# Optimization experiments

Hardware: AMD Instinct MI355X
Metric: run time of the kernel (lower is better)

The kernel has to match this reference:

```python
import jax, jax.numpy as jnp
import numpy as np

KC = 32      # cluster_num
KS = 3       # kernel_size
AREA = KS * KS
ITERS = 10   # KMeans Lloyd iterations (fixed, deterministic init)


def _unfold3(x):
    # torch nn.Unfold(kernel_size=3, padding=1): feature dim ordered cin-major, area-minor
    b, c, h, w = x.shape
    xp = jnp.pad(x, ((0, 0), (0, 0), (1, 1), (1, 1)))
    cols = jnp.stack([xp[:, :, i:i + h, j:j + w] for i in range(KS) for j in range(KS)], axis=2)  # [b,c,area,h,w]
    return cols.reshape(b, c * AREA, h * w).transpose(0, 2, 1)  # [b, hw, c*area]


def _kmeans_assign(feat):
    # Lloyd's KMeans on [s, d] features; deterministic strided init; returns [s] int assignments
    s, d = feat.shape
    c0 = feat[jnp.arange(KC) * (s // KC)]
    f2 = (feat * feat).sum(-1, keepdims=True)
    def dists(c):
        return f2 - 2.0 * feat @ c.T + (c * c).sum(-1)[None, :]
    def step(c, _):
        idx = jnp.argmin(dists(c), axis=1)
        cnt = jax.ops.segment_sum(jnp.ones((s,), feat.dtype), idx, KC)
        sm = jax.ops.segment_sum(feat, idx, KC)
        c_new = jnp.where(cnt[:, None] > 0, sm / jnp.maximum(cnt, 1.0)[:, None], c)
        return c_new, None
    c, _ = jax.lax.scan(step, c0, None, length=ITERS)
    return jnp.argmin(dists(c), axis=1)


def _seg_mean(p, idx):
    # per-cluster mean of patches -> patch-space centroids [K, f]
    s = p.shape[0]
    cnt = jax.ops.segment_sum(jnp.ones((s,), p.dtype), idx, KC)
    return jax.ops.segment_sum(p, idx, KC) / jnp.maximum(cnt, 1.0)[:, None]


def _mlp2(x, W1, b1, W2, b2):
    return jax.nn.relu(jax.nn.relu(x @ W1 + b1) @ W2 + b2)


def setup_inputs():
    key = jax.random.key(0)
    ks = jax.random.split(key, 16)
    cin, cout, m = 32, 32, 16
    f = cin * AREA
    g = lambda k, shp, sc: jax.random.normal(k, shp, dtype=jnp.float32) * sc
    return {
        "x": g(ks[0], (4, cin, 64, 64), 1.0),
        "Wh1": g(ks[1], (f, m), (2.0 / f) ** 0.5), "bh1": jnp.zeros((m,), jnp.float32),
        "Wh2": g(ks[2], (m, m), (2.0 / m) ** 0.5), "bh2": jnp.zeros((m,), jnp.float32),
        "Wa": g(ks[3], (m, AREA), (2.0 / m) ** 0.5), "ba": jnp.zeros((AREA,), jnp.float32),
        "Wc": g(ks[4], (m, cin), (2.0 / m) ** 0.5), "bc": jnp.zeros((cin,), jnp.float32),
        "Wo": g(ks[5], (m, cout), (2.0 / m) ** 0.5), "bo": jnp.zeros((cout,), jnp.float32),
        "kernels": g(ks[6], (cin, AREA, cout), (2.0 / (cin * AREA)) ** 0.5),
        "Wb1": g(ks[7], (f, m), (2.0 / f) ** 0.5), "bb1": jnp.zeros((m,), jnp.float32),
        "Wb2": g(ks[8], (m, m), (2.0 / m) ** 0.5), "bb2": jnp.zeros((m,), jnp.float32),
        "Wb3": g(ks[9], (m, cout), (2.0 / m) ** 0.5), "bb3": jnp.zeros((cout,), jnp.float32),
    }


def reference(x, Wh1, bh1, Wh2, bh2, Wa, ba, Wc, bc, Wo, bo, kernels, Wb1, bb1, Wb2, bb2, Wb3, bb3):
    b, cin, h, w = x.shape
    s = h * w
    cout = kernels.shape[-1]
    patches = _unfold3(x)                                        # [b, s, cin*area]
    feat = patches.reshape(b, s, cin, AREA).mean(-1)             # cluster_source='channel'
    idx = jax.vmap(_kmeans_assign)(jax.lax.stop_gradient(feat))  # [b, s] cluster assignments
    centroids = jax.vmap(_seg_mean)(patches, idx)                # [b, K, cin*area]
    # low_rank kernel generator: rank-1 modulation along cin/area/cout of shared base kernel
    kf = _mlp2(centroids, Wh1, bh1, Wh2, bh2)                    # [b, K, m]
    w_cin = jax.nn.sigmoid(kf @ Wc + bc)                         # [b, K, cin]
    w_area = jax.nn.sigmoid(kf @ Wa + ba)                        # [b, K, area]
    w_cout = jax.nn.sigmoid(kf @ Wo + bo)                        # [b, K, cout]
    kern = (w_cin[:, :, :, None, None] * w_area[:, :, None, :, None]
            * w_cout[:, :, None, None, :] * kernels[None, None])  # [b, K, cin, area, cout]
    kern = kern.reshape(b, KC, cin * AREA, cout)
    bias = _mlp2(centroids, Wb1, bb1, Wb2, bb2) @ Wb3 + bb3      # [b, K, cout] (bias='cluster')
    # gather per-pixel kernel/bias by cluster id, grouped matmul, scatter back (dense-gather form)
    bi = jnp.arange(b)[:, None]
    Wpix = kern[bi, idx]                                         # [b, s, f, cout]
    out = jnp.einsum('bsf,bsfo->bso', patches, Wpix) + bias[bi, idx]
    return out.reshape(b, h, w, cout).transpose(0, 3, 1, 2), idx
```

## Files before the change

### kernel.cpp

```cpp
#include <hip/hip_runtime.h>
#include <stdint.h>

typedef unsigned long long u64;

#define Bn 4
#define CINn 32
#define Hn 64
#define Wn 64
#define Sn 4096
#define KCn 32
#define Mn 16
#define COUTn 32
#define AREAn 9
#define Fn 288
#define NITER 10
#define FXSCALE 4294967296.0
#define NBLK_B 16
#define PXB 256
#define CMAX 160
#define LDK 292
#define NFLAG ((NITER + 2) * Bn * NBLK_B)

#define AT_LD_U32(p)    __hip_atomic_load((p),  __ATOMIC_RELAXED, __HIP_MEMORY_SCOPE_AGENT)
#define AT_LD_U64(p)    __hip_atomic_load((p),  __ATOMIC_RELAXED, __HIP_MEMORY_SCOPE_AGENT)
#define AT_ST_U32(p,v)  __hip_atomic_store((p), (v), __ATOMIC_RELAXED, __HIP_MEMORY_SCOPE_AGENT)
#define AT_ST_U64(p,v)  __hip_atomic_store((p), (v), __ATOMIC_RELAXED, __HIP_MEMORY_SCOPE_AGENT)

static __device__ __forceinline__ float relu_(float v){ return v > 0.f ? v : 0.f; }
static __device__ __forceinline__ float sigmoid_(float v){ return 1.f / (1.f + expf(-v)); }

__global__ __launch_bounds__(256) void k_init(const float* __restrict__ x,
                                              float* __restrict__ feat,
                                              u64* __restrict__ gsum,
                                              unsigned* __restrict__ gcnt,
                                              unsigned* __restrict__ flags){
    int g = blockIdx.x * 256 + threadIdx.x;
    if (g < 3 * Bn * KCn * CINn) gsum[g] = 0ull;
    if (g < 3 * Bn * KCn)        gcnt[g] = 0u;
    if (g < NFLAG)               flags[g] = 0u;
    int p = g & (Sn - 1);
    int c = (g >> 12) & (CINn - 1);
    int b = g >> 17;
    int y = p >> 6, xx = p & 63;
    const float* xc = x + ((size_t)(b * CINn + c) << 12);
    float s = 0.f;
    #pragma unroll
    for (int i = 0; i < 3; ++i){
        int yy = y + i - 1;
        if (yy < 0 || yy >= Hn) continue;
        #pragma unroll
        for (int j = 0; j < 3; ++j){
            int xj = xx + j - 1;
            if (xj < 0 || xj >= Wn) continue;
            s += xc[(yy << 6) + xj];
        }
    }
    feat[g] = s * (1.f / 9.f);
}

struct AssignSh {
    float4 fvQ[8][PXB];
    float  f2L[PXB];
    float4 cent4[KCn][8];
    float  c2[KCn];
    float  bestdM[4][PXB];
    int    bestkM[4][PXB];
    unsigned lcnt[KCn];
    unsigned off32[KCn + 1];
    unsigned scat[KCn];
    unsigned cntPrev[KCn];
    int   plist[PXB];
    int   rankF[PXB];
    unsigned baseBT[KCn];
};
struct SmkSh {
    float psum[CINn][AREAn][8];
    float centL[Fn];
    int   pl[256];
    float part1[16][16], part2[16][16];
    float hL[2][Mn];
    float kfL[2][Mn];
};
union ShU { AssignSh a; SmkSh m; };

__global__ __launch_bounds__(256) void k_main(const float* __restrict__ x,
        const float* __restrict__ feat,
        u64* __restrict__ gsum, unsigned* __restrict__ gcnt,
        unsigned* __restrict__ blkcnt,
        int* __restrict__ idx, float* __restrict__ idxf,
        int* __restrict__ sorted, int4* __restrict__ chunk_map,
        const float* __restrict__ Wh1, const float* __restrict__ bh1,
        const float* __restrict__ Wh2, const float* __restrict__ bh2,
        const float* __restrict__ Wa,  const float* __restrict__ ba,
        const float* __restrict__ Wc,  const float* __restrict__ bc,
        const float* __restrict__ Wo,  const float* __restrict__ bo,
        const float* __restrict__ Wb1, const float* __restrict__ bb1,
        const float* __restrict__ Wb2, const float* __restrict__ bb2,
        const float* __restrict__ Wb3, const float* __restrict__ bb3,
        float* __restrict__ wcin, float* __restrict__ warea,
        float* __restrict__ wcout, float* __restrict__ biasb,
        unsigned* __restrict__ flg){
    __shared__ int bi256[PXB];
    __shared__ unsigned totK[KCn];
    __shared__ unsigned goffK[KCn + 1];
    __shared__ ShU sh;

    const int tid  = threadIdx.x;
    const int b    = blockIdx.x >> 4;
    const int tnum = blockIdx.x & 15;
    const int p    = tnum * PXB + tid;
    const int kq   = tid >> 6;
    const int pxb  = tid & 63;

    #pragma unroll
    for (int cq = 0; cq < 8; ++cq){
        float4 v;
        v.x = feat[(b * CINn + cq * 4 + 0) * Sn + p];
        v.y = feat[(b * CINn + cq * 4 + 1) * Sn + p];
        v.z = feat[(b * CINn + cq * 4 + 2) * Sn + p];
        v.w = feat[(b * CINn + cq * 4 + 3) * Sn + p];
        sh.a.fvQ[cq][tid] = v;
    }
    __syncthreads();
    {
        float s = 0.f;
        #pragma unroll
        for (int cq = 0; cq < 8; ++cq){
            float4 v = sh.a.fvQ[cq][tid];
            s = fmaf(v.x, v.x, s); s = fmaf(v.y, v.y, s);
            s = fmaf(v.z, v.z, s); s = fmaf(v.w, v.w, s);
        }
        sh.a.f2L[tid] = s;
    }

    for (int iter = 0; iter <= NITER; ++iter){
        const int prev = (iter + 2) % 3;
        const int cur  = iter % 3;
        const int nxt  = (iter + 1) % 3;

        if (iter == 0){
            float* centf = (float*)sh.a.cent4;
            for (int e = tid; e < KCn * CINn; e += 256){
                int k = e >> 5, c = e & 31;
                centf[k * 32 + c] = feat[(b * CINn + c) * Sn + k * (Sn / KCn)];
            }
        } else {
            if (tid < NBLK_B)
                while (AT_LD_U32(&flg[(iter - 1) * Bn * NBLK_B + b * NBLK_B + tid]) == 0u)
                    __builtin_amdgcn_s_sleep(2);
            __syncthreads();
            if (tid < KCn)
                sh.a.cntPrev[tid] = AT_LD_U32(&gcnt[(prev * Bn + b) * KCn + tid]);
            u64 sv[4];
            #pragma unroll
            for (int q = 0; q < 4; ++q)
                sv[q] = AT_LD_U64(&gsum[(size_t)(prev * Bn + b) * KCn * CINn + tid + q * 256]);
            __syncthreads();
            float* centf = (float*)sh.a.cent4;
            #pragma unroll
            for (int q = 0; q < 4; ++q){
                int e = tid + q * 256;
                int k = e >> 5, c = e & 31;
                unsigned cn = sh.a.cntPrev[k];
                if (cn > 0)
                    centf[k * 32 + c] = (float)((double)(long long)sv[q] / ((double)cn * FXSCALE));
            }
        }
        if (iter < NITER && tnum == 0){
            for (int e = tid; e < KCn * CINn; e += 256)
                AT_ST_U64(&gsum[(size_t)(nxt * Bn + b) * KCn * CINn + e], 0ull);
            if (tid < KCn) AT_ST_U32(&gcnt[(nxt * Bn + b) * KCn + tid], 0u);
        }
        __syncthreads();
        if (tid < KCn){
            const float4* cr = sh.a.cent4[tid];
            float s = 0.f;
            #pragma unroll
            for (int cq2 = 0; cq2 < 8; ++cq2){
                float4 v = cr[cq2];
                s = fmaf(v.x, v.x, s); s = fmaf(v.y, v.y, s);
                s = fmaf(v.z, v.z, s); s = fmaf(v.w, v.w, s);
            }
            sh.a.c2[tid] = s;
            sh.a.lcnt[tid] = 0u;
            sh.a.scat[tid] = 0u;
        }
        __syncthreads();

        float dot[4][8];
        #pragma unroll
        for (int j = 0; j < 4; ++j)
            #pragma unroll
            for (int kk = 0; kk < 8; ++kk) dot[j][kk] = 0.f;
        #pragma unroll
        for (int cq2 = 0; cq2 < 8; ++cq2){
            float4 fr0 = sh.a.fvQ[cq2][pxb];
            float4 fr1 = sh.a.fvQ[cq2][pxb + 64];
            float4 fr2 = sh.a.fvQ[cq2][pxb + 128];
            float4 fr3 = sh.a.fvQ[cq2][pxb + 192];
            #pragma unroll
            for (int kk = 0; kk < 8; ++kk){
                float4 cv = sh.a.cent4[kq * 8 + kk][cq2];
                dot[0][kk] = fmaf(fr0.x, cv.x, dot[0][kk]); dot[0][kk] = fmaf(fr0.y, cv.y, dot[0][kk]);
                dot[0][kk] = fmaf(fr0.z, cv.z, dot[0][kk]); dot[0][kk] = fmaf(fr0.w, cv.w, dot[0][kk]);
                dot[1][kk] = fmaf(fr1.x, cv.x, dot[1][kk]); dot[1][kk] = fmaf(fr1.y, cv.y, dot[1][kk]);
                dot[1][kk] = fmaf(fr1.z, cv.z, dot[1][kk]); dot[1][kk] = fmaf(fr1.w, cv.w, dot[1][kk]);
                dot[2][kk] = fmaf(fr2.x, cv.x, dot[2][kk]); dot[2][kk] = fmaf(fr2.y, cv.y, dot[2][kk]);
                dot[2][kk] = fmaf(fr2.z, cv.z, dot[2][kk]); dot[2][kk] = fmaf(fr2.w, cv.w, dot[2][kk]);
                dot[3][kk] = fmaf(fr3.x, cv.x, dot[3][kk]); dot[3][kk] = fmaf(fr3.y, cv.y, dot[3][kk]);
                dot[3][kk] = fmaf(fr3.z, cv.z, dot[3][kk]); dot[3][kk] = fmaf(fr3.w, cv.w, dot[3][kk]);
            }
        }
        #pragma unroll
        for (int j = 0; j < 4; ++j){
            const int px = pxb + 64 * j;
            const float f2v = sh.a.f2L[px];
            float bd = 3.402823466e38f; int bkk = kq * 8;
            #pragma unroll
            for (int kk = 0; kk < 8; ++kk){
                float d = f2v - 2.f * dot[j][kk] + sh.a.c2[kq * 8 + kk];
                if (d < bd){ bd = d; bkk = kq * 8 + kk; }
            }
            sh.a.bestdM[kq][px] = bd;
            sh.a.bestkM[kq][px] = bkk;
        }
        __syncthreads();
        int bk;
        {
            float bd = sh.a.bestdM[0][tid]; bk = sh.a.bestkM[0][tid];
            #pragma unroll
            for (int q = 1; q < 4; ++q){
                float d2 = sh.a.bestdM[q][tid];
                if (d2 < bd){ bd = d2; bk = sh.a.bestkM[q][tid]; }
            }
            bi256[tid] = bk;
        }

        if (iter < NITER){
            atomicAdd(&sh.a.lcnt[bk], 1u);
            __syncthreads();
            if (tid == 0){
                unsigned acc = 0;
                #pragma unroll
                for (int k = 0; k < KCn; ++k){ sh.a.off32[k] = acc; acc += sh.a.lcnt[k]; }
                sh.a.off32[KCn] = acc;
            }
            __syncthreads();
            {
                unsigned pos = sh.a.off32[bk] + atomicAdd(&sh.a.scat[bk], 1u);
                sh.a.plist[pos] = tid;
            }
            __syncthreads();
            {
                const int wv   = tid >> 6;
                const int lane = tid & 63;
                const int hf   = lane >> 5;
                const int c    = lane & 31;
                const float* fvf = (const float*)sh.a.fvQ;
                #pragma unroll
                for (int kq2 = 0; kq2 < 8; ++kq2){
                    const int k  = wv * 8 + kq2;
                    const int o0 = (int)sh.a.off32[k];
                    const int n  = (int)sh.a.off32[k + 1] - o0;
                    u64 acc = 0ull;
                    for (int i = hf; i < n; i += 2){
                        int px = sh.a.plist[o0 + i];
                        float fvv = fvf[(c >> 2) * 1024 + px * 4 + (c & 3)];
                        acc += (u64)llrint((double)fvv * FXSCALE);
                    }
                    acc += __shfl_down(acc, 32);
                    if (lane < 32 && n > 0)
                        atomicAdd(&gsum[(size_t)(cur * Bn + b) * KCn * CINn + k * CINn + c], acc);
                }
            }
            if (tid < KCn){
                unsigned v = sh.a.lcnt[tid];
                if (v) atomicAdd(&gcnt[(cur * Bn + b) * KCn + tid], v);
            }
            __syncthreads();
            if (tid == 0)
                AT_ST_U32(&flg[iter * Bn * NBLK_B + b * NBLK_B + tnum], 1u);
        } else {
            idx [b * Sn + p] = bk;
            idxf[b * Sn + p] = (float)bk;
            __syncthreads();
            if (tid < KCn){
                int r = 0;
                for (int q = 0; q < PXB; ++q)
                    if (bi256[q] == tid) sh.a.rankF[q] = r++;
                AT_ST_U32(&blkcnt[(b * KCn + tid) * NBLK_B + tnum], (unsigned)r);
            }
            __syncthreads();
            if (tid == 0)
                AT_ST_U32(&flg[NITER * Bn * NBLK_B + b * NBLK_B + tnum], 1u);
        }
    }

    if (tid < NBLK_B)
        while (AT_LD_U32(&flg[NITER * Bn * NBLK_B + b * NBLK_B + tid]) == 0u)
            __builtin_amdgcn_s_sleep(2);
    __syncthreads();
    if (tid < KCn){
        unsigned run = 0, mybase = 0;
        #pragma unroll 4
        for (int blk = 0; blk < NBLK_B; ++blk){
            unsigned v = AT_LD_U32(&blkcnt[(b * KCn + tid) * NBLK_B + blk]);
            if (blk == tnum) mybase = run;
            run += v;
        }
        totK[tid] = run;
        sh.a.baseBT[tid] = mybase;
    }
    __syncthreads();
    if (tid == 0){
        unsigned acc = 0;
        #pragma unroll
        for (int k = 0; k < KCn; ++k){ goffK[k] = acc; acc += totK[k]; }
        goffK[KCn] = acc;
    }
    __syncthreads();
    {
        int k = bi256[tid];
        unsigned pos = goffK[k] + sh.a.baseBT[k] + (unsigned)sh.a.rankF[tid];
        AT_ST_U32((unsigned*)&sorted[b * Sn + pos], (unsigned)p);
    }
    if (tnum == 0 && tid == 0){
        int j = 0;
        for (int k = 0; k < KCn; ++k){
            int n = (int)totK[k];
            for (int cb = 0; cb < n; cb += 32){
                chunk_map[b * CMAX + j] = make_int4(k, (int)goffK[k] + cb, min(32, n - cb), 0);
                ++j;
            }
        }
        for (; j < CMAX; ++j) chunk_map[b * CMAX + j] = make_int4(-1, 0, 0, 0);
    }
    __syncthreads();
    if (tid == 0)
        AT_ST_U32(&flg[(NITER + 1) * Bn * NBLK_B + b * NBLK_B + tnum], 1u);
    if (tid < NBLK_B)
        while (AT_LD_U32(&flg[(NITER + 1) * Bn * NBLK_B + b * NBLK_B + tid]) == 0u)
            __builtin_amdgcn_s_sleep(2);
    __syncthreads();

    for (int kq2 = 0; kq2 < 2; ++kq2){
        const int kk   = tnum * 2 + kq2;
        const int off0 = (int)goffK[kk];
        const int nmy  = (int)totK[kk];
        __syncthreads();
        {
            const int cA = tid >> 3;
            const int s  = tid & 7;
            const float* xc = x + ((size_t)(b * CINn + cA) << 12);
            float acc[9];
            #pragma unroll
            for (int a = 0; a < 9; ++a) acc[a] = 0.f;
            for (int base = 0; base < nmy; base += 256){
                int m = min(256, nmy - base);
                __syncthreads();
                if (tid < m)
                    sh.m.pl[tid] = (int)AT_LD_U32((unsigned*)&sorted[b * Sn + off0 + base + tid]);
                __syncthreads();
                #pragma unroll 2
                for (int i = s; i < m; i += 8){
                    int pp = sh.m.pl[i];
                    int py = pp >> 6, px2 = pp & 63;
                    #pragma unroll
                    for (int a = 0; a < 9; ++a){
                        int y1 = py + a / 3 - 1, x1 = px2 + (a % 3) - 1;
                        float v = (y1 >= 0 && y1 < Hn && x1 >= 0 && x1 < Wn)
                                  ? xc[(y1 << 6) + x1] : 0.f;
                        acc[a] += v;
                    }
                }
            }
            __syncthreads();
            #pragma unroll
            for (int a = 0; a < 9; ++a) sh.m.psum[cA][a][s] = acc[a];
            __syncthreads();
            float invn = 1.f / (float)max(nmy, 1);
            for (int f = tid; f < Fn; f += 256){
                int c = f / 9, a = f - c * 9;
                float sm = 0.f;
                #pragma unroll
                for (int s2 = 0; s2 < 8; ++s2) sm += sh.m.psum[c][a][s2];
                sh.m.centL[f] = sm * invn;
            }
        }
        __syncthreads();
        {
            int j = tid & 15, rep = tid >> 4;
            float p1 = 0.f, p2 = 0.f;
            int fbeg = rep * 18;
            for (int ff = fbeg; ff < fbeg + 18; ++ff){
                float cv = sh.m.centL[ff];
                p1 = fmaf(cv, Wh1[ff * Mn + j], p1);
                p2 = fmaf(cv, Wb1[ff * Mn + j], p2);
            }
            sh.m.part1[rep][j] = p1;
            sh.m.part2[rep][j] = p2;
        }
        __syncthreads();
        if (tid < 32){
            int br = tid >> 4, j = tid & 15;
            float s = br ? bb1[j] : bh1[j];
            for (int r = 0; r < 16; ++r) s += br ? sh.m.part2[r][j] : sh.m.part1[r][j];
            sh.m.hL[br][j] = relu_(s);
        }
        __syncthreads();
        if (tid < 32){
            int br = tid >> 4, j = tid & 15;
            const float* W2 = br ? Wb2 : Wh2;
            float s = br ? bb2[j] : bh2[j];
            #pragma unroll
            for (int i = 0; i < Mn; ++i) s = fmaf(sh.m.hL[br][i], W2[i * Mn + j], s);
            sh.m.kfL[br][j] = relu_(s);
        }
        __syncthreads();
        if (tid < 32){
            int o = tid;
            float s1 = bc[o], s2 = bo[o], s3 = bb3[o];
            #pragma unroll
            for (int i = 0; i < Mn; ++i){
                float kv = sh.m.kfL[0][i];
                s1 = fmaf(kv, Wc[i * COUTn + o], s1);
                s2 = fmaf(kv, Wo[i * COUTn + o], s2);
                s3 = fmaf(sh.m.kfL[1][i], Wb3[i * COUTn + o], s3);
            }
            wcin [(b * KCn + kk) * CINn  + o] = sigmoid_(s1);
            wcout[(b * KCn + kk) * COUTn + o] = sigmoid_(s2);
            biasb[(b * KCn + kk) * COUTn + o] = s3;
        } else if (tid < 41){
            int a2 = tid - 32;
            float s = ba[a2];
            #pragma unroll
            for (int i = 0; i < Mn; ++i) s = fmaf(sh.m.kfL[0][i], Wa[i * AREAn + a2], s);
            warea[(b * KCn + kk) * AREAn + a2] = sigmoid_(s);
        }
    }
}

__global__ __launch_bounds__(256) void k_out(const float* __restrict__ x,
                                             const int* __restrict__ sorted,
                                             const int4* __restrict__ chunk_map,
                                             const float* __restrict__ wcin,
                                             const float* __restrict__ warea,
                                             const float* __restrict__ wcout,
                                             const float* __restrict__ biasb,
                                             const float* __restrict__ kern0,
                                             float* __restrict__ out){
    const int b   = blockIdx.x / CMAX;
    const int j   = blockIdx.x - b * CMAX;
    const int tid = threadIdx.x;

    int4 cm = chunk_map[b * CMAX + j];
    const int kcur = cm.x;
    if (kcur < 0) return;
    const int base = cm.y;
    const int cnt  = cm.z;

    __shared__ float kernT[COUTn * LDK];
    __shared__ float patchL[32 * LDK];
    __shared__ int   pix[32];
    __shared__ float wcl[CINn], wal[AREAn], wol[COUTn], biasL[COUTn];

    if (tid < 32){
        pix[tid] = (tid < cnt) ? sorted[b * Sn + base + tid] : -1;
    } else if (tid < 64)  wcl[tid - 32]    = wcin [(b * KCn + kcur) * CINn  + tid - 32];
    else if (tid < 96)    wol[tid - 64]    = wcout[(b * KCn + kcur) * COUTn + tid - 64];
    else if (tid < 105)   wal[tid - 96]    = warea[(b * KCn + kcur) * AREAn + tid - 96];
    else if (tid >= 128 && tid < 160) biasL[tid - 128] = biasb[(b * KCn + kcur) * COUTn + tid - 128];

    const int fA = tid;       const int cA = fA / 9, aA = fA - cA * 9;
    const int dyA = aA / 3 - 1, dxA = aA % 3 - 1;
    const int fB = 256 + tid; const int cB = fB / 9, aB = fB - cB * 9;
    const int dyB = aB / 3 - 1, dxB = aB % 3 - 1;
    __syncthreads();

    {
        int o  = tid >> 3;
        int q  = tid & 7;
        int f0 = q * 36;
        int cc = q * 4, aa = 0;
        float wo_ = wol[o];
        float* kr = kernT + o * LDK + f0;
        #pragma unroll 4
        for (int i2 = 0; i2 < 36; ++i2){
            kr[i2] = wcl[cc] * wal[aa] * wo_ * kern0[(f0 + i2) * COUTn + o];
            if (++aa == 9){ aa = 0; ++cc; }
        }
    }

    #pragma unroll 4
    for (int px = 0; px < 32; ++px){
        int pp = pix[px];
        float vA = 0.f, vB = 0.f;
        if (pp >= 0){
            int py = pp >> 6, pxx = pp & 63;
            int y1 = py + dyA, x1 = pxx + dxA;
            if (y1 >= 0 && y1 < Hn && x1 >= 0 && x1 < Wn)
                vA = x[((size_t)(b * CINn + cA) << 12) + (y1 << 6) + x1];
            if (tid < 32){
                int y2 = py + dyB, x2 = pxx + dxB;
                if (y2 >= 0 && y2 < Hn && x2 >= 0 && x2 < Wn)
                    vB = x[((size_t)(b * CINn + cB) << 12) + (y2 << 6) + x2];
            }
        }
        patchL[px * LDK + tid] = vA;
        if (tid < 32) patchL[px * LDK + 256 + tid] = vB;
    }
    __syncthreads();

    const int o2 = tid & 15, p2 = tid >> 4;
    const int oA = o2 * 2, oB = o2 * 2 + 1;
    const int pxA = p2 * 2, pxB = p2 * 2 + 1;
    const bool actA = pxA < cnt, actB = pxB < cnt;
    if (!actA && !actB) return;

    const float* krA = kernT + oA * LDK;
    const float* krB = kernT + oB * LDK;
    const float* prA = patchL + pxA * LDK;
    const float* prB = patchL + pxB * LDK;
    float s00 = 0.f, s01 = 0.f, s10 = 0.f, s11 = 0.f;
    #pragma unroll 4
    for (int fq = 0; fq < Fn; fq += 4){
        float4 k0 = *reinterpret_cast<const float4*>(krA + fq);
        float4 k1 = *reinterpret_cast<const float4*>(krB + fq);
        float4 pa = *reinterpret_cast<const float4*>(prA + fq);
        float4 pb = *reinterpret_cast<const float4*>(prB + fq);
        s00 = fmaf(pa.x,k0.x,s00); s00 = fmaf(pa.y,k0.y,s00); s00 = fmaf(pa.z,k0.z,s00); s00 = fmaf(pa.w,k0.w,s00);
        s01 = fmaf(pa.x,k1.x,s01); s01 = fmaf(pa.y,k1.y,s01); s01 = fmaf(pa.z,k1.z,s01); s01 = fmaf(pa.w,k1.w,s01);
        s10 = fmaf(pb.x,k0.x,s10); s10 = fmaf(pb.y,k0.y,s10); s10 = fmaf(pb.z,k0.z,s10); s10 = fmaf(pb.w,k0.w,s10);
        s11 = fmaf(pb.x,k1.x,s11); s11 = fmaf(pb.y,k1.y,s11); s11 = fmaf(pb.z,k1.z,s11); s11 = fmaf(pb.w,k1.w,s11);
    }
    if (actA){
        int pp = pix[pxA];
        out[((size_t)(b * COUTn + oA) << 12) + pp] = biasL[oA] + s00;
        out[((size_t)(b * COUTn + oB) << 12) + pp] = biasL[oB] + s01;
    }
    if (actB){
        int pp = pix[pxB];
        out[((size_t)(b * COUTn + oA) << 12) + pp] = biasL[oA] + s10;
        out[((size_t)(b * COUTn + oB) << 12) + pp] = biasL[oB] + s11;
    }
}

extern "C" void kernel_launch(void* const* d_in, const int* in_sizes, int n_in,
                              void* d_out, int out_size, void* d_ws, size_t ws_size,
                              hipStream_t stream){
    const float* x    = (const float*)d_in[0];
    const float* Wh1  = (const float*)d_in[1];
    const float* bh1  = (const float*)d_in[2];
    const float* Wh2  = (const float*)d_in[3];
    const float* bh2  = (const float*)d_in[4];
    const float* Wa   = (const float*)d_in[5];
    const float* ba   = (const float*)d_in[6];
    const float* Wc   = (const float*)d_in[7];
    const float* bc   = (const float*)d_in[8];
    const float* Wo   = (const float*)d_in[9];
    const float* bo   = (const float*)d_in[10];
    const float* kern0= (const float*)d_in[11];
    const float* Wb1  = (const float*)d_in[12];
    const float* bb1  = (const float*)d_in[13];
    const float* Wb2  = (const float*)d_in[14];
    const float* bb2  = (const float*)d_in[15];
    const float* Wb3  = (const float*)d_in[16];
    const float* bb3  = (const float*)d_in[17];

    char* ws = (char*)d_ws;
    float*    feat   = (float*)(ws + 0);
    u64*      gsum   = (u64*)  (ws + 2097152);
    unsigned* gcnt   = (unsigned*)(ws + 2195456);
    unsigned* blkcnt = (unsigned*)(ws + 2196992);
    int*      idx    = (int*)  (ws + 2205184);
    int*      sorted = (int*)  (ws + 2270720);
    float*    wcin   = (float*)(ws + 2336256);
    float*    warea  = (float*)(ws + 2352640);
    float*    wcout  = (float*)(ws + 2357248);
    float*    biasb  = (float*)(ws + 2373632);
    int4*     chunk_map = (int4*)(ws + 2390016);
    unsigned* flags  = (unsigned*)(ws + 2400256);

    float* outp = (float*)d_out;
    float* idxf = outp + (size_t)Bn * COUTn * Sn;

    k_init<<<(Bn * CINn * Sn) / 256, 256, 0, stream>>>(x, feat, gsum, gcnt, flags);
    k_main<<<Bn * NBLK_B, 256, 0, stream>>>(x, feat, gsum, gcnt, blkcnt, idx, idxf,
                                            sorted, chunk_map,
                                            Wh1, bh1, Wh2, bh2, Wa, ba, Wc, bc, Wo, bo,
                                            Wb1, bb1, Wb2, bb2, Wb3, bb3,
                                            wcin, warea, wcout, biasb, flags);
    k_out<<<Bn * CMAX, 256, 0, stream>>>(x, sorted, chunk_map, wcin, warea, wcout,
                                         biasb, kern0, outp);
}
```

Before: 230.9 us.

## Replace global atomics with per-block slots and leader-reduced centroids in KMeans loop

KMeans partial sums are no longer atomically added into shared global accumulators. Each block now writes its own slot, and block 0 of each batch reduces the slots, computes the centroids and their norms, then publishes them behind a flag for the other blocks. Patch-space centroid sums are load-balanced by splitting sorted pixel runs across all blocks, with float atomics into a global buffer. The change also adds a padded transposed feature copy in LDS to avoid bank conflicts, and changes the output tile thread mapping. This removes atomic contention, but adds an extra serial leader step and an extra barrier per iteration, and float atomics make the result order-dependent.

```diff
diff --git a/kernel.cpp b/kernel.cpp
--- a/kernel.cpp
+++ b/kernel.cpp
@@ -19,7 +19,13 @@
 #define PXB 256
 #define CMAX 160
 #define LDK 292
-#define NFLAG ((NITER + 2) * Bn * NBLK_B)
+
+#define FL_PUB(it)  ((it)*64)
+#define FL_CENT(it) (640 + (it)*4)
+#define FL_SORT  680
+#define FL_SCAT  744
+#define FL_SEG   808
+#define NFLAGS   1024
 
 #define AT_LD_U32(p)    __hip_atomic_load((p),  __ATOMIC_RELAXED, __HIP_MEMORY_SCOPE_AGENT)
 #define AT_LD_U64(p)    __hip_atomic_load((p),  __ATOMIC_RELAXED, __HIP_MEMORY_SCOPE_AGENT)
@@ -31,13 +37,11 @@
 
 __global__ __launch_bounds__(256) void k_init(const float* __restrict__ x,
                                               float* __restrict__ feat,
-                                              u64* __restrict__ gsum,
-                                              unsigned* __restrict__ gcnt,
+                                              float* __restrict__ gpsum,
                                               unsigned* __restrict__ flags){
     int g = blockIdx.x * 256 + threadIdx.x;
-    if (g < 3 * Bn * KCn * CINn) gsum[g] = 0ull;
-    if (g < 3 * Bn * KCn)        gcnt[g] = 0u;
-    if (g < NFLAG)               flags[g] = 0u;
+    if (g < Bn * KCn * Fn) gpsum[g] = 0.f;
+    if (g < NFLAGS)        flags[g] = 0u;
     int p = g & (Sn - 1);
     int c = (g >> 12) & (CINn - 1);
     int b = g >> 17;
@@ -60,6 +64,7 @@
 
 struct AssignSh {
     float4 fvQ[8][PXB];
+    float  fvP[PXB][33];
     float  f2L[PXB];
     float4 cent4[KCn][8];
     float  c2[KCn];
@@ -68,15 +73,17 @@
     unsigned lcnt[KCn];
     unsigned off32[KCn + 1];
     unsigned scat[KCn];
-    unsigned cntPrev[KCn];
-    int   plist[PXB];
-    int   rankF[PXB];
+    unsigned cntTot[KCn];
+    int    plist[PXB];
+    int    rankF[PXB];
     unsigned baseBT[KCn];
 };
 struct SmkSh {
     float psum[CINn][AREAn][8];
     float centL[Fn];
-    int   pl[256];
+    int   spl[PXB];
+    int   runK[33], runS[33], runE[33];
+    int   nruns;
     float part1[16][16], part2[16][16];
     float hL[2][Mn];
     float kfL[2][Mn];
@@ -85,9 +92,10 @@
 
 __global__ __launch_bounds__(256) void k_main(const float* __restrict__ x,
         const float* __restrict__ feat,
-        u64* __restrict__ gsum, unsigned* __restrict__ gcnt,
+        u64* __restrict__ bslot, unsigned* __restrict__ slotCnt,
+        float* __restrict__ centG, float* __restrict__ c2G,
         unsigned* __restrict__ blkcnt,
-        int* __restrict__ idx, float* __restrict__ idxf,
+        float* __restrict__ idxf,
         int* __restrict__ sorted, int4* __restrict__ chunk_map,
         const float* __restrict__ Wh1, const float* __restrict__ bh1,
         const float* __restrict__ Wh2, const float* __restrict__ bh2,
@@ -99,6 +107,7 @@
         const float* __restrict__ Wb3, const float* __restrict__ bb3,
         float* __restrict__ wcin, float* __restrict__ warea,
         float* __restrict__ wcout, float* __restrict__ biasb,
+        float* __restrict__ gpsum,
         unsigned* __restrict__ flg){
     __shared__ int bi256[PXB];
     __shared__ unsigned totK[KCn];
@@ -112,6 +121,7 @@
     const int kq   = tid >> 6;
     const int pxb  = tid & 63;
 
+    float fv[CINn];
     #pragma unroll
     for (int cq = 0; cq < 8; ++cq){
         float4 v;
@@ -120,71 +130,99 @@
         v.z = feat[(b * CINn + cq * 4 + 2) * Sn + p];
         v.w = feat[(b * CINn + cq * 4 + 3) * Sn + p];
         sh.a.fvQ[cq][tid] = v;
-    }
-    __syncthreads();
+        fv[cq * 4 + 0] = v.x; fv[cq * 4 + 1] = v.y;
+        fv[cq * 4 + 2] = v.z; fv[cq * 4 + 3] = v.w;
+    }
     {
         float s = 0.f;
         #pragma unroll
-        for (int cq = 0; cq < 8; ++cq){
-            float4 v = sh.a.fvQ[cq][tid];
-            s = fmaf(v.x, v.x, s); s = fmaf(v.y, v.y, s);
-            s = fmaf(v.z, v.z, s); s = fmaf(v.w, v.w, s);
-        }
+        for (int c = 0; c < CINn; ++c) s = fmaf(fv[c], fv[c], s);
         sh.a.f2L[tid] = s;
-    }
+        #pragma unroll
+        for (int c = 0; c < CINn; ++c) sh.a.fvP[tid][c] = fv[c];
+    }
+    __syncthreads();
 
     for (int iter = 0; iter <= NITER; ++iter){
-        const int prev = (iter + 2) % 3;
-        const int cur  = iter % 3;
-        const int nxt  = (iter + 1) % 3;
-
         if (iter == 0){
             float* centf = (float*)sh.a.cent4;
             for (int e = tid; e < KCn * CINn; e += 256){
                 int k = e >> 5, c = e & 31;
-                centf[k * 32 + c] = feat[(b * CINn + c) * Sn + k * (Sn / KCn)];
-            }
+                centf[e] = feat[(b * CINn + c) * Sn + k * (Sn / KCn)];
+            }
+            __syncthreads();
+            if (tid < KCn){
+                const float4* cr = sh.a.cent4[tid];
+                float s = 0.f;
+                #pragma unroll
+                for (int cq2 = 0; cq2 < 8; ++cq2){
+                    float4 v = cr[cq2];
+                    s = fmaf(v.x, v.x, s); s = fmaf(v.y, v.y, s);
+                    s = fmaf(v.z, v.z, s); s = fmaf(v.w, v.w, s);
+                }
+                sh.a.c2[tid] = s;
+            }
+        } else if (tnum == 0){
+            if (tid < NBLK_B)
+                while (AT_LD_U32(&flg[FL_PUB(iter - 1) + b * 16 + tid]) == 0u)
+                    __builtin_amdgcn_s_sleep(2);
+            __syncthreads();
+            u64 s4[4] = {0ull, 0ull, 0ull, 0ull};
+            #pragma unroll
+            for (int q = 0; q < 4; ++q){
+                const int e = tid + q * 256;
+                #pragma unroll
+                for (int blk = 0; blk < NBLK_B; ++blk)
+                    s4[q] += AT_LD_U64(&bslot[(size_t)(b * NBLK_B + blk) * 1024 + e]);
+            }
+            if (tid < KCn){
+                unsigned ct = 0;
+                #pragma unroll
+                for (int blk = 0; blk < NBLK_B; ++blk)
+                    ct += AT_LD_U32(&slotCnt[(b * NBLK_B + blk) * KCn + tid]);
+                sh.a.cntTot[tid] = ct;
+            }
+            __syncthreads();
+            float* centf = (float*)sh.a.cent4;
+            #pragma unroll
+            for (int q = 0; q < 4; ++q){
+                const int e = tid + q * 256;
+                const int k = e >> 5;
+                unsigned cn = sh.a.cntTot[k];
+                if (cn > 0)
+                    centf[e] = (float)((double)(long long)s4[q] / ((double)cn * FXSCALE));
+                AT_ST_U32((unsigned*)&centG[b * 1024 + e], __float_as_uint(centf[e]));
+            }
+            __syncthreads();
+            if (tid < KCn){
+                const float4* cr = sh.a.cent4[tid];
+                float s = 0.f;
+                #pragma unroll
+                for (int cq2 = 0; cq2 < 8; ++cq2){
+                    float4 v = cr[cq2];
+                    s = fmaf(v.x, v.x, s); s = fmaf(v.y, v.y, s);
+                    s = fmaf(v.z, v.z, s); s = fmaf(v.w, v.w, s);
+                }
+                sh.a.c2[tid] = s;
+                AT_ST_U32((unsigned*)&c2G[b * KCn + tid], __float_as_uint(s));
+            }
+            __syncthreads();
+            if (tid == 0) AT_ST_U32(&flg[FL_CENT(iter - 1) + b], 1u);
         } else {
-            if (tid < NBLK_B)
-                while (AT_LD_U32(&flg[(iter - 1) * Bn * NBLK_B + b * NBLK_B + tid]) == 0u)
+            if (tid == 0)
+                while (AT_LD_U32(&flg[FL_CENT(iter - 1) + b]) == 0u)
                     __builtin_amdgcn_s_sleep(2);
             __syncthreads();
+            float* centf = (float*)sh.a.cent4;
+            #pragma unroll
+            for (int q = 0; q < 4; ++q){
+                const int e = tid + q * 256;
+                centf[e] = __uint_as_float(AT_LD_U32((unsigned*)&centG[b * 1024 + e]));
+            }
             if (tid < KCn)
-                sh.a.cntPrev[tid] = AT_LD_U32(&gcnt[(prev * Bn + b) * KCn + tid]);
-            u64 sv[4];
-            #pragma unroll
-            for (int q = 0; q < 4; ++q)
-                sv[q] = AT_LD_U64(&gsum[(size_t)(prev * Bn + b) * KCn * CINn + tid + q * 256]);
-            __syncthreads();
-            float* centf = (float*)sh.a.cent4;
-            #pragma unroll
-            for (int q = 0; q < 4; ++q){
-                int e = tid + q * 256;
-                int k = e >> 5, c = e & 31;
-                unsigned cn = sh.a.cntPrev[k];
-                if (cn > 0)
-                    centf[k * 32 + c] = (float)((double)(long long)sv[q] / ((double)cn * FXSCALE));
-            }
-        }
-        if (iter < NITER && tnum == 0){
-            for (int e = tid; e < KCn * CINn; e += 256)
-                AT_ST_U64(&gsum[(size_t)(nxt * Bn + b) * KCn * CINn + e], 0ull);
-            if (tid < KCn) AT_ST_U32(&gcnt[(nxt * Bn + b) * KCn + tid], 0u);
-        }
-        __syncthreads();
-        if (tid < KCn){
-            const float4* cr = sh.a.cent4[tid];
-            float s = 0.f;
-            #pragma unroll
-            for (int cq2 = 0; cq2 < 8; ++cq2){
-                float4 v = cr[cq2];
-                s = fmaf(v.x, v.x, s); s = fmaf(v.y, v.y, s);
-                s = fmaf(v.z, v.z, s); s = fmaf(v.w, v.w, s);
-            }
-            sh.a.c2[tid] = s;
-            sh.a.lcnt[tid] = 0u;
-            sh.a.scat[tid] = 0u;
-        }
+                sh.a.c2[tid] = __uint_as_float(AT_LD_U32((unsigned*)&c2G[b * KCn + tid]));
+        }
+        if (tid < KCn){ sh.a.lcnt[tid] = 0u; sh.a.scat[tid] = 0u; }
         __syncthreads();
 
         float dot[4][8];
@@ -256,7 +294,6 @@
                 const int lane = tid & 63;
                 const int hf   = lane >> 5;
                 const int c    = lane & 31;
-                const float* fvf = (const float*)sh.a.fvQ;
                 #pragma unroll
                 for (int kq2 = 0; kq2 < 8; ++kq2){
                     const int k  = wv * 8 + kq2;
@@ -265,23 +302,18 @@
                     u64 acc = 0ull;
                     for (int i = hf; i < n; i += 2){
                         int px = sh.a.plist[o0 + i];
-                        float fvv = fvf[(c >> 2) * 1024 + px * 4 + (c & 3)];
-                        acc += (u64)llrint((double)fvv * FXSCALE);
+                        acc += (u64)llrint((double)sh.a.fvP[px][c] * FXSCALE);
                     }
                     acc += __shfl_down(acc, 32);
-                    if (lane < 32 && n > 0)
-                        atomicAdd(&gsum[(size_t)(cur * Bn + b) * KCn * CINn + k * CINn + c], acc);
+                    if (lane < 32)
+                        AT_ST_U64(&bslot[(size_t)(b * NBLK_B + tnum) * 1024 + k * 32 + c], acc);
                 }
             }
-            if (tid < KCn){
-                unsigned v = sh.a.lcnt[tid];
-                if (v) atomicAdd(&gcnt[(cur * Bn + b) * KCn + tid], v);
-            }
-            __syncthreads();
-            if (tid == 0)
-                AT_ST_U32(&flg[iter * Bn * NBLK_B + b * NBLK_B + tnum], 1u);
+            if (tid < KCn)
+                AT_ST_U32(&slotCnt[(b * NBLK_B + tnum) * KCn + tid], sh.a.lcnt[tid]);
+            __syncthreads();
+            if (tid == 0) AT_ST_U32(&flg[FL_PUB(iter) + b * 16 + tnum], 1u);
         } else {
-            idx [b * Sn + p] = bk;
             idxf[b * Sn + p] = (float)bk;
             __syncthreads();
             if (tid < KCn){
@@ -291,13 +323,12 @@
                 AT_ST_U32(&blkcnt[(b * KCn + tid) * NBLK_B + tnum], (unsigned)r);
             }
             __syncthreads();
-            if (tid == 0)
-                AT_ST_U32(&flg[NITER * Bn * NBLK_B + b * NBLK_B + tnum], 1u);
+            if (tid == 0) AT_ST_U32(&flg[FL_SORT + b * 16 + tnum], 1u);
         }
     }
 
     if (tid < NBLK_B)
-        while (AT_LD_U32(&flg[NITER * Bn * NBLK_B + b * NBLK_B + tid]) == 0u)
+        while (AT_LD_U32(&flg[FL_SORT + b * 16 + tid]) == 0u)
             __builtin_amdgcn_s_sleep(2);
     __syncthreads();
     if (tid < KCn){
@@ -322,7 +353,7 @@
     {
         int k = bi256[tid];
         unsigned pos = goffK[k] + sh.a.baseBT[k] + (unsigned)sh.a.rankF[tid];
-        AT_ST_U32((unsigned*)&sorted[b * Sn + pos], (unsigned)p);
+        AT_ST_U32((unsigned*)&sorted[b * Sn + pos], (unsigned)(p | (k << 16)));
     }
     if (tnum == 0 && tid == 0){
         int j = 0;
@@ -336,57 +367,84 @@
         for (; j < CMAX; ++j) chunk_map[b * CMAX + j] = make_int4(-1, 0, 0, 0);
     }
     __syncthreads();
-    if (tid == 0)
-        AT_ST_U32(&flg[(NITER + 1) * Bn * NBLK_B + b * NBLK_B + tnum], 1u);
+    if (tid == 0) AT_ST_U32(&flg[FL_SCAT + b * 16 + tnum], 1u);
     if (tid < NBLK_B)
-        while (AT_LD_U32(&flg[(NITER + 1) * Bn * NBLK_B + b * NBLK_B + tid]) == 0u)
+        while (AT_LD_U32(&flg[FL_SCAT + b * 16 + tid]) == 0u)
             __builtin_amdgcn_s_sleep(2);
     __syncthreads();
 
-    for (int kq2 = 0; kq2 < 2; ++kq2){
-        const int kk   = tnum * 2 + kq2;
-        const int off0 = (int)goffK[kk];
-        const int nmy  = (int)totK[kk];
-        __syncthreads();
-        {
-            const int cA = tid >> 3;
-            const int s  = tid & 7;
-            const float* xc = x + ((size_t)(b * CINn + cA) << 12);
+    {
+        sh.m.spl[tid] = (int)AT_LD_U32((unsigned*)&sorted[b * Sn + tnum * PXB + tid]);
+        __syncthreads();
+        if (tid == 0){
+            int nr = 0, s0 = 0, kcur = sh.m.spl[0] >> 16;
+            for (int i = 1; i < PXB; ++i){
+                int kx = sh.m.spl[i] >> 16;
+                if (kx != kcur){
+                    sh.m.runK[nr] = kcur; sh.m.runS[nr] = s0; sh.m.runE[nr] = i;
+                    ++nr; kcur = kx; s0 = i;
+                }
+            }
+            sh.m.runK[nr] = kcur; sh.m.runS[nr] = s0; sh.m.runE[nr] = PXB;
+            sh.m.nruns = nr + 1;
+        }
+        __syncthreads();
+        const int cc = tid >> 3;
+        const int sl = tid & 7;
+        const float* xc = x + ((size_t)(b * CINn + cc) << 12);
+        const int nruns = sh.m.nruns;
+        for (int r = 0; r < nruns; ++r){
+            const int ks = sh.m.runK[r];
+            const int i0 = sh.m.runS[r], i1 = sh.m.runE[r];
             float acc[9];
             #pragma unroll
             for (int a = 0; a < 9; ++a) acc[a] = 0.f;
-            for (int base = 0; base < nmy; base += 256){
-                int m = min(256, nmy - base);
-                __syncthreads();
-                if (tid < m)
-                    sh.m.pl[tid] = (int)AT_LD_U32((unsigned*)&sorted[b * Sn + off0 + base + tid]);
-                __syncthreads();
-                #pragma unroll 2
-                for (int i = s; i < m; i += 8){
-                    int pp = sh.m.pl[i];
-                    int py = pp >> 6, px2 = pp & 63;
-                    #pragma unroll
-                    for (int a = 0; a < 9; ++a){
-                        int y1 = py + a / 3 - 1, x1 = px2 + (a % 3) - 1;
-                        float v = (y1 >= 0 && y1 < Hn && x1 >= 0 && x1 < Wn)
-                                  ? xc[(y1 << 6) + x1] : 0.f;
-                        acc[a] += v;
-                    }
+            for (int i = i0 + sl; i < i1; i += 8){
+                int pp = sh.m.spl[i] & 0xFFFF;
+                int py = pp >> 6, px2 = pp & 63;
+                #pragma unroll
+                for (int a = 0; a < 9; ++a){
+                    int y1 = py + a / 3 - 1, x1 = px2 + (a % 3) - 1;
+                    float v = (y1 >= 0 && y1 < Hn && x1 >= 0 && x1 < Wn)
+                              ? xc[(y1 << 6) + x1] : 0.f;
+                    acc[a] += v;
                 }
             }
-            __syncthreads();
-            #pragma unroll
-            for (int a = 0; a < 9; ++a) sh.m.psum[cA][a][s] = acc[a];
-            __syncthreads();
-            float invn = 1.f / (float)max(nmy, 1);
-            for (int f = tid; f < Fn; f += 256){
+            #pragma unroll
+            for (int a = 0; a < 9; ++a) sh.m.psum[cc][a][sl] = acc[a];
+            __syncthreads();
+            {
+                int f = tid;
                 int c = f / 9, a = f - c * 9;
                 float sm = 0.f;
                 #pragma unroll
                 for (int s2 = 0; s2 < 8; ++s2) sm += sh.m.psum[c][a][s2];
-                sh.m.centL[f] = sm * invn;
-            }
-        }
+                atomicAdd(&gpsum[((size_t)b * KCn + ks) * Fn + f], sm);
+                if (tid < 32){
+                    int f2i = 256 + tid;
+                    int c2i = f2i / 9, a2i = f2i - c2i * 9;
+                    float sm2 = 0.f;
+                    #pragma unroll
+                    for (int s2 = 0; s2 < 8; ++s2) sm2 += sh.m.psum[c2i][a2i][s2];
+                    atomicAdd(&gpsum[((size_t)b * KCn + ks) * Fn + f2i], sm2);
+                }
+            }
+            __syncthreads();
+        }
+    }
+    __syncthreads();
+    if (tid == 0) AT_ST_U32(&flg[FL_SEG + b * 16 + tnum], 1u);
+    if (tid < NBLK_B)
+        while (AT_LD_U32(&flg[FL_SEG + b * 16 + tid]) == 0u)
+            __builtin_amdgcn_s_sleep(2);
+    __syncthreads();
+
+    for (int kq2 = 0; kq2 < 2; ++kq2){
+        const int kk = tnum * 2 + kq2;
+        const float invn = 1.f / (float)max(totK[kk], 1u);
+        __syncthreads();
+        for (int f = tid; f < Fn; f += 256)
+            sh.m.centL[f] = __uint_as_float(AT_LD_U32((unsigned*)&gpsum[((size_t)b * KCn + kk) * Fn + f])) * invn;
         __syncthreads();
         {
             int j = tid & 15, rep = tid >> 4;
@@ -465,7 +523,7 @@
     __shared__ float wcl[CINn], wal[AREAn], wol[COUTn], biasL[COUTn];
 
     if (tid < 32){
-        pix[tid] = (tid < cnt) ? sorted[b * Sn + base + tid] : -1;
+        pix[tid] = (tid < cnt) ? (sorted[b * Sn + base + tid] & 0xFFFF) : -1;
     } else if (tid < 64)  wcl[tid - 32]    = wcin [(b * KCn + kcur) * CINn  + tid - 32];
     else if (tid < 96)    wol[tid - 64]    = wcout[(b * KCn + kcur) * COUTn + tid - 64];
     else if (tid < 105)   wal[tid - 96]    = warea[(b * KCn + kcur) * AREAn + tid - 96];
@@ -512,8 +570,8 @@
     __syncthreads();
 
     const int o2 = tid & 15, p2 = tid >> 4;
-    const int oA = o2 * 2, oB = o2 * 2 + 1;
-    const int pxA = p2 * 2, pxB = p2 * 2 + 1;
+    const int oA = o2, oB = o2 + 16;
+    const int pxA = p2, pxB = p2 + 16;
     const bool actA = pxA < cnt, actB = pxB < cnt;
     if (!actA && !actB) return;
 
@@ -568,28 +626,30 @@
     const float* bb3  = (const float*)d_in[17];
 
     char* ws = (char*)d_ws;
-    float*    feat   = (float*)(ws + 0);
-    u64*      gsum   = (u64*)  (ws + 2097152);
-    unsigned* gcnt   = (unsigned*)(ws + 2195456);
-    unsigned* blkcnt = (unsigned*)(ws + 2196992);
-    int*      idx    = (int*)  (ws + 2205184);
-    int*      sorted = (int*)  (ws + 2270720);
-    float*    wcin   = (float*)(ws + 2336256);
-    float*    warea  = (float*)(ws + 2352640);
-    float*    wcout  = (float*)(ws + 2357248);
-    float*    biasb  = (float*)(ws + 2373632);
-    int4*     chunk_map = (int4*)(ws + 2390016);
-    unsigned* flags  = (unsigned*)(ws + 2400256);
+    float*    feat    = (float*)(ws + 0);
+    u64*      bslot   = (u64*)  (ws + 2097152);
+    unsigned* slotCnt = (unsigned*)(ws + 2621440);
+    float*    centG   = (float*)(ws + 2629632);
+    float*    c2G     = (float*)(ws + 2646016);
+    unsigned* blkcnt  = (unsigned*)(ws + 2646528);
+    int*      sorted  = (int*)  (ws + 2654720);
+    float*    gpsum   = (float*)(ws + 2720256);
+    float*    wcin    = (float*)(ws + 2867712);
+    float*    warea   = (float*)(ws + 2884096);
+    float*    wcout   = (float*)(ws + 2888704);
+    float*    biasb   = (float*)(ws + 2905088);
+    int4*     chunk_map = (int4*)(ws + 2921472);
+    unsigned* flags   = (unsigned*)(ws + 2931712);
 
     float* outp = (float*)d_out;
     float* idxf = outp + (size_t)Bn * COUTn * Sn;
 
-    k_init<<<(Bn * CINn * Sn) / 256, 256, 0, stream>>>(x, feat, gsum, gcnt, flags);
-    k_main<<<Bn * NBLK_B, 256, 0, stream>>>(x, feat, gsum, gcnt, blkcnt, idx, idxf,
-                                            sorted, chunk_map,
+    k_init<<<(Bn * CINn * Sn) / 256, 256, 0, stream>>>(x, feat, gpsum, flags);
+    k_main<<<Bn * NBLK_B, 256, 0, stream>>>(x, feat, bslot, slotCnt, centG, c2G,
+                                            blkcnt, idxf, sorted, chunk_map,
                                             Wh1, bh1, Wh2, bh2, Wa, ba, Wc, bc, Wo, bo,
                                             Wb1, bb1, Wb2, bb2, Wb3, bb3,
-                                            wcin, warea, wcout, biasb, flags);
+                                            wcin, warea, wcout, biasb, gpsum, flags);
     k_out<<<Bn * CMAX, 256, 0, stream>>>(x, sorted, chunk_map, wcin, warea, wcout,
                                          biasb, kern0, outp);
 }
```

Result: slower. 287.7 us (+24.6%).
